# Kernel tuning notes

Measured on AMD Instinct MI355X. Metric: run time of the kernel, lower is better.

## Reference

```python
import jax, jax.numpy as jnp
import numpy as np

N_NODES = 50000
N_EDGES = 800000
F_IN = 11
HID = 128
HEADS = 4
N_ACT = 6
NEG_SLOPE = 0.2


def _gat_layer(x, W, a_src, a_dst, b, src, dst, heads, out_dim):
    # x: [N, Fin]; W: [Fin, heads*out]; a_src/a_dst: [heads, out]; b: [heads*out]
    N = x.shape[0]
    h = (x @ W).reshape(N, heads, out_dim)                     # [N,H,C]
    alpha_src = jnp.einsum('nhc,hc->nh', h, a_src)             # [N,H]
    alpha_dst = jnp.einsum('nhc,hc->nh', h, a_dst)             # [N,H]
    e = jax.nn.leaky_relu(alpha_src[src] + alpha_dst[dst], NEG_SLOPE)  # [E,H]
    # segment softmax over incoming edges of each dst node
    m = jax.ops.segment_max(e, dst, num_segments=N)            # [N,H]
    ex = jnp.exp(e - m[dst])
    s = jax.ops.segment_sum(ex, dst, num_segments=N)           # [N,H]
    alpha = ex / s[dst]                                        # [E,H]
    msg = h[src] * alpha[..., None]                            # [E,H,C]
    agg = jax.ops.segment_sum(msg, dst, num_segments=N)        # [N,H,C]
    return agg.reshape(N, heads * out_dim) + b


def setup_inputs() -> dict:
    key = jax.random.key(0)
    ks = jax.random.split(key, 24)
    f32 = jnp.float32
    p = {}
    p['x'] = jax.random.normal(ks[0], (N_NODES, F_IN), dtype=f32)
    p['edge_index'] = jax.random.randint(ks[1], (2, N_EDGES), 0, N_NODES, dtype=jnp.int64)
    p['current_node_idx'] = 0
    def w(k, shape):
        return (jax.random.normal(k, shape, dtype=f32) * 0.1)
    p['W1'] = w(ks[2], (F_IN, HEADS * HID)); p['as1'] = w(ks[3], (HEADS, HID))
    p['ad1'] = w(ks[4], (HEADS, HID)); p['b1'] = jnp.zeros((HEADS * HID,), f32)
    p['W2'] = w(ks[5], (HEADS * HID, HEADS * HID)); p['as2'] = w(ks[6], (HEADS, HID))
    p['ad2'] = w(ks[7], (HEADS, HID)); p['b2'] = jnp.zeros((HEADS * HID,), f32)
    # layer 3: 512 -> 128, 1 head
    p['W3'] = w(ks[8], (HEADS * HID, HID)); p['as3'] = w(ks[9], (1, HID))
    p['ad3'] = w(ks[10], (1, HID)); p['b3'] = jnp.zeros((HID,), f32)
    # policy head
    p['pw1'] = w(ks[11], (HID, HID)); p['pb1'] = jnp.zeros((HID,), f32)
    p['pw2'] = w(ks[12], (HID, N_ACT)); p['pb2'] = jnp.zeros((N_ACT,), f32)
    # value head
    p['vw1'] = w(ks[13], (HID, HID)); p['vb1'] = jnp.zeros((HID,), f32)
    p['vw2'] = w(ks[14], (HID, 1)); p['vb2'] = jnp.zeros((1,), f32)
    return p


def reference(x, edge_index, current_node_idx,
              W1, as1, ad1, b1, W2, as2, ad2, b2, W3, as3, ad3, b3,
              pw1, pb1, pw2, pb2, vw1, vb1, vw2, vb2):
    src, dst = edge_index[0], edge_index[1]
    h = _gat_layer(x, W1, as1, ad1, b1, src, dst, HEADS, HID)
    h = jax.nn.elu(h)
    h = _gat_layer(h, W2, as2, ad2, b2, src, dst, HEADS, HID)
    h = jax.nn.elu(h)
    h = _gat_layer(h, W3, as3, ad3, b3, src, dst, 1, HID)      # [N, HID]
    graph_emb = h.mean(axis=0, keepdims=True)                  # [1, HID]
    combined = graph_emb + h[current_node_idx]                 # [1, HID]
    p = jax.nn.relu(combined @ pw1 + pb1) @ pw2 + pb2          # [1, N_ACT]
    v = jax.nn.relu(combined @ vw1 + vb1) @ vw2 + vb2          # [1, 1]
    return p, v
```

## Files before the change

kernel.cpp:

```cpp
#include <hip/hip_runtime.h>
#include <math.h>

#define NN 50000
#define NE 800000
#define F_IN 11
#define HID 128
#define NEG_SLOPE 0.2f

typedef __attribute__((ext_vector_type(8))) short short8;
typedef __attribute__((ext_vector_type(4))) float f32x4;

__device__ __forceinline__ float bf2f(ushort u) {
  return __uint_as_float(((unsigned)u) << 16);
}
__device__ __forceinline__ ushort f2bf(float f) {
  unsigned u = __float_as_uint(f);
  return (ushort)((u + 0x7fff + ((u >> 16) & 1)) >> 16);
}
__device__ __forceinline__ float lrelu(float x) { return x > 0.f ? x : NEG_SLOPE * x; }
__device__ __forceinline__ float elu1(float x) { return x > 0.f ? x : expm1f(x); }

#define MNEG (-1e30f)

__device__ __forceinline__ void wave_fence() {
  asm volatile("s_waitcnt lgkmcnt(0)" ::: "memory");
}

#define AS1 __attribute__((address_space(1)))
#define AS3 __attribute__((address_space(3)))

__global__ void k_deg(const int* __restrict__ ei, int* __restrict__ deg) {
  int e = blockIdx.x * blockDim.x + threadIdx.x;
  if (e < NE) atomicAdd(&deg[ei[NE + e]], 1);
}

__global__ void k_scan(const int* __restrict__ deg, int* __restrict__ row_ptr,
                       int* __restrict__ cursor) {
  const int T = 1024;
  const int CH = (NN + T - 1) / T;
  __shared__ int ssum[T];
  int t = threadIdx.x;
  int base = t * CH;
  int s = 0;
  for (int i = 0; i < CH; i++) {
    int idx = base + i;
    if (idx < NN) s += deg[idx];
  }
  ssum[t] = s;
  __syncthreads();
  for (int off = 1; off < T; off <<= 1) {
    int v = (t >= off) ? ssum[t - off] : 0;
    __syncthreads();
    ssum[t] += v;
    __syncthreads();
  }
  int run = ssum[t] - s;
  for (int i = 0; i < CH; i++) {
    int idx = base + i;
    if (idx < NN) {
      row_ptr[idx] = run;
      cursor[idx] = run;
      run += deg[idx];
    }
  }
  if (t == 0) row_ptr[NN] = ssum[T - 1];
}

__global__ void k_scatter(const int* __restrict__ ei, int* __restrict__ cursor,
                          int* __restrict__ csr_src) {
  int e = blockIdx.x * blockDim.x + threadIdx.x;
  if (e < NE) {
    int d = ei[NE + e];
    int pos = atomicAdd(&cursor[d], 1);
    csr_src[pos] = ei[e];
  }
}

__global__ void k_wt(const float* __restrict__ W, ushort* __restrict__ Wt, int K, int N) {
  __shared__ float tl[32][33];
  int bn = blockIdx.x * 32, bk = blockIdx.y * 32;
  int tx = threadIdx.x & 31, ty = threadIdx.x >> 5;
  for (int i = ty; i < 32; i += 8) tl[i][tx] = W[(size_t)(bk + i) * N + bn + tx];
  __syncthreads();
  for (int i = ty; i < 32; i += 8)
    Wt[(size_t)(bn + i) * K + bk + tx] = f2bf(tl[tx][i]);
}

__global__ void k_vsd(const float* __restrict__ W1, const float* __restrict__ as1,
                      const float* __restrict__ ad1, float* __restrict__ vs,
                      float* __restrict__ vd) {
  int t = threadIdx.x;
  if (t >= 88) return;
  int side = t & 1, kh = t >> 1;
  int k = kh >> 2, h = kh & 3;
  const float* av = side ? ad1 : as1;
  float s = 0.f;
  for (int c = 0; c < HID; c++) s += W1[k * 512 + h * HID + c] * av[h * HID + c];
  (side ? vd : vs)[kh] = s;
}

__global__ void k_ax(const float* __restrict__ x, const float* __restrict__ vs,
                     const float* __restrict__ vd, float* __restrict__ asrc,
                     float* __restrict__ adst) {
  int n = blockIdx.x * blockDim.x + threadIdx.x;
  if (n >= NN) return;
  float xr[F_IN];
#pragma unroll
  for (int k = 0; k < F_IN; k++) xr[k] = x[n * F_IN + k];
  float s[4] = {}, dd[4] = {};
#pragma unroll
  for (int k = 0; k < F_IN; k++)
#pragma unroll
    for (int h = 0; h < 4; h++) {
      s[h] += xr[k] * vs[k * 4 + h];
      dd[h] += xr[k] * vd[k * 4 + h];
    }
  *(f32x4*)(asrc + n * 4) = f32x4{s[0], s[1], s[2], s[3]};
  *(f32x4*)(adst + n * 4) = f32x4{dd[0], dd[1], dd[2], dd[3]};
}

__global__ __launch_bounds__(256) void k_aggpre(
    const float* __restrict__ x, const float* __restrict__ asrc,
    const float* __restrict__ adst, const int* __restrict__ row_ptr,
    const int* __restrict__ csr_src, float* __restrict__ P) {
  const int CAP = 64;
  __shared__ int src_c[4][CAP];
  __shared__ float ea[4][CAP * 4];
  int t = threadIdx.x, lane = t & 63, wv = t >> 6;
  int d = blockIdx.x * 4 + wv;
  int start = row_ptr[d], deg = row_ptr[d + 1] - start;
  int dcap = min(deg, CAP);
  for (int i = lane; i < dcap; i += 64) src_c[wv][i] = csr_src[start + i];
  wave_fence();
  int hh = lane & 3;
  float adh = adst[d * 4 + hh];
  float m = MNEG, s = 0.f;
  int deg4 = deg * 4;
  for (int i = lane; i < deg4; i += 64) {
    int k = i >> 2;
    int sn = (k < CAP) ? src_c[wv][k] : csr_src[start + k];
    float v = lrelu(asrc[sn * 4 + hh] + adh);
    if (k < CAP) ea[wv][i] = v;
    float nm = fmaxf(m, v);
    s = s * __expf(m - nm) + __expf(v - nm);
    m = nm;
  }
#pragma unroll
  for (int off = 4; off < 64; off <<= 1) {
    float m2 = __shfl_xor(m, off);
    float s2 = __shfl_xor(s, off);
    float nm = fmaxf(m, m2);
    s = s * __expf(m - nm) + s2 * __expf(m2 - nm);
    m = nm;
  }
  float sinv = (s > 0.f) ? 1.f / s : 0.f;
  int dc4 = dcap * 4;
  for (int i = lane; i < dc4; i += 64) ea[wv][i] = __expf(ea[wv][i] - m) * sinv;
  wave_fence();
  int hq = lane / F_IN;
  int k = lane - hq * F_IN;
  int h = hq & 3;
  float mh = __shfl(m, h), sih = __shfl(sinv, h);
  float adh2 = adst[d * 4 + h];
  float acc = 0.f;
#define GETP(i, SN, A)                                                \
  do {                                                                \
    int kk_ = e + (i);                                                \
    if (kk_ < CAP) {                                                  \
      SN = src_c[wv][kk_];                                            \
      A = ea[wv][kk_ * 4 + h];                                        \
    } else {                                                          \
      SN = csr_src[start + kk_];                                      \
      A = __expf(lrelu(asrc[SN * 4 + h] + adh2) - mh) * sih;          \
    }                                                                 \
  } while (0)
  int e = 0;
  for (; e + 4 <= deg; e += 4) {
    int sn0, sn1, sn2, sn3;
    float a0, a1, a2, a3;
    GETP(0, sn0, a0);
    GETP(1, sn1, a1);
    GETP(2, sn2, a2);
    GETP(3, sn3, a3);
    float x0 = x[sn0 * F_IN + k];
    float x1 = x[sn1 * F_IN + k];
    float x2 = x[sn2 * F_IN + k];
    float x3 = x[sn3 * F_IN + k];
    acc += a0 * x0 + a1 * x1 + a2 * x2 + a3 * x3;
  }
  for (; e < deg; e++) {
    int sn;
    float a;
    GETP(0, sn, a);
    acc += a * x[sn * F_IN + k];
  }
#undef GETP
  if (lane < 44) P[(size_t)d * 44 + lane] = acc;
}

__global__ __launch_bounds__(256) void k_gemm_l1(
    const float* __restrict__ P, const float* __restrict__ W1,
    const float* __restrict__ b1, ushort* __restrict__ out) {
  __shared__ float sW[F_IN * 512];
  __shared__ float sP[64][44];
  int t = threadIdx.x;
  for (int i = t; i < F_IN * 512; i += 256) sW[i] = W1[i];
  int n0 = blockIdx.x * 64;
  for (int i = t; i < 64 * 44; i += 256) {
    int nn = i / 44, kk = i % 44;
    sP[nn][kk] = (n0 + nn < NN) ? P[(size_t)(n0 + nn) * 44 + kk] : 0.f;
  }
  __syncthreads();
  int j0 = 2 * t;
  int h = j0 >> 7;
  float b0 = b1[j0], bb = b1[j0 + 1];
  float w0[F_IN], w1v[F_IN];
#pragma unroll
  for (int k = 0; k < F_IN; k++) {
    w0[k] = sW[k * 512 + j0];
    w1v[k] = sW[k * 512 + j0 + 1];
  }
  for (int nn = 0; nn < 64; nn++) {
    if (n0 + nn >= NN) break;
    float a0 = b0, a1 = bb;
#pragma unroll
    for (int k = 0; k < F_IN; k++) {
      float pv = sP[nn][h * F_IN + k];
      a0 += pv * w0[k];
      a1 += pv * w1v[k];
    }
    a0 = elu1(a0);
    a1 = elu1(a1);
    unsigned pk = (unsigned)f2bf(a0) | ((unsigned)f2bf(a1) << 16);
    *(unsigned*)(out + (size_t)(n0 + nn) * 512 + j0) = pk;
  }
}

#define TM 128
#define TN 128
#define TK 64
__global__ __launch_bounds__(256) void k_mfma(const ushort* __restrict__ A,
                                              const ushort* __restrict__ Bt,
                                              ushort* __restrict__ C,
                                              int M, int N, int K, int H) {
  __shared__ ushort lds[TM * TK + TN * TK];
  ushort* As = lds;
  ushort* Bs = lds + TM * TK;
  int tid = threadIdx.x;
  int lane = tid & 63, wv = tid >> 6;
  int wr = wv >> 1, wc = wv & 1;
  int nwg = gridDim.x;
  int q = nwg >> 3, rr = nwg & 7;
  int xcd = blockIdx.x & 7, off8 = blockIdx.x >> 3;
  int lid = (xcd < rr ? xcd * (q + 1) : rr * (q + 1) + (xcd - rr) * q) + off8;
  int bm = lid / H, hy = lid - bm * H;
  int bm0 = bm * TM, bn0 = hy * TN;
  int l15 = lane & 15, l4 = lane >> 4;
  f32x4 acc[4][4] = {};
  for (int k0 = 0; k0 < K; k0 += TK) {
#pragma unroll
    for (int it = 0; it < 4; ++it) {
      int chunk = it * 4 + wv;
      int pbase = chunk * 1024;
      int p = pbase + lane * 16;
      int prow = p >> 7;
      int lblk = ((p >> 4) & 7) ^ (prow & 7);
      int gr = bm0 + prow;
      gr = gr < M ? gr : M - 1;
      __builtin_amdgcn_global_load_lds(
          (const AS1 void*)(A + (size_t)gr * K + (k0 + lblk * 8)),
          (AS3 void*)((char*)As + pbase), 16, 0, 0);
      int gb = bn0 + prow;
      __builtin_amdgcn_global_load_lds(
          (const AS1 void*)(Bt + (size_t)gb * K + (k0 + lblk * 8)),
          (AS3 void*)((char*)Bs + pbase), 16, 0, 0);
    }
    __syncthreads();
#pragma unroll
    for (int kk = 0; kk < 2; ++kk) {
      int cb = kk * 4 + l4;
      short8 af[4], bfr[4];
#pragma unroll
      for (int m = 0; m < 4; ++m) {
        int row = wr * 64 + m * 16 + l15;
        af[m] = *(const short8*)((const char*)As + row * 128 + ((cb ^ (row & 7)) << 4));
      }
#pragma unroll
      for (int n = 0; n < 4; ++n) {
        int row = wc * 64 + n * 16 + l15;
        bfr[n] = *(const short8*)((const char*)Bs + row * 128 + ((cb ^ (row & 7)) << 4));
      }
#pragma unroll
      for (int m = 0; m < 4; ++m)
#pragma unroll
        for (int n = 0; n < 4; ++n)
          acc[m][n] = __builtin_amdgcn_mfma_f32_16x16x32_bf16(af[m], bfr[n], acc[m][n], 0, 0, 0);
    }
    __syncthreads();
  }
#pragma unroll
  for (int m = 0; m < 4; ++m) {
#pragma unroll
    for (int r = 0; r < 4; ++r) {
      int row = bm0 + wr * 64 + m * 16 + l4 * 4 + r;
      if (row < M) {
#pragma unroll
        for (int n = 0; n < 4; ++n) {
          int col = bn0 + wc * 64 + n * 16 + l15;
          C[(size_t)row * N + col] = f2bf(acc[m][n][r]);
        }
      }
    }
  }
}

template <int H>
__global__ void k_alpha(const ushort* __restrict__ h, const float* __restrict__ a_src,
                        const float* __restrict__ a_dst, float* __restrict__ asrc,
                        float* __restrict__ adst) {
  int t = threadIdx.x;
  int lane = t & 63;
  int n_g, h_g;
  if (H == 4) {
    n_g = blockIdx.x * 4 + (t >> 6);
    h_g = lane >> 4;
  } else {
    n_g = blockIdx.x * 16 + (t >> 4);
    h_g = 0;
  }
  if (n_g >= NN) return;
  int cl = lane & 15;
  short8 hv = *(const short8*)(h + (size_t)n_g * (H * 128) + h_g * 128 + cl * 8);
  const float* as = a_src + h_g * 128 + cl * 8;
  const float* ad = a_dst + h_g * 128 + cl * 8;
  float s1 = 0.f, s2 = 0.f;
#pragma unroll
  for (int j = 0; j < 8; j++) {
    float v = bf2f((ushort)hv[j]);
    s1 += v * as[j];
    s2 += v * ad[j];
  }
#pragma unroll
  for (int off = 1; off < 16; off <<= 1) {
    s1 += __shfl_xor(s1, off);
    s2 += __shfl_xor(s2, off);
  }
  if (cl == 0) {
    asrc[n_g * H + h_g] = s1;
    adst[n_g * H + h_g] = s2;
  }
}

__global__ __launch_bounds__(256) void k_agg4w(
    const ushort* __restrict__ h, const float* __restrict__ asrc,
    const float* __restrict__ adst, const int* __restrict__ row_ptr,
    const int* __restrict__ csr_src, const float* __restrict__ bias,
    ushort* __restrict__ out) {
  const int CAP = 64;
  __shared__ int src_c[4][CAP];
  __shared__ float ea[4][CAP * 4];
  int t = threadIdx.x, lane = t & 63, wv = t >> 6;
  int d = blockIdx.x * 4 + wv;
  int start = row_ptr[d], deg = row_ptr[d + 1] - start;
  int dcap = min(deg, CAP);
  for (int i = lane; i < dcap; i += 64) src_c[wv][i] = csr_src[start + i];
  wave_fence();
  int hh = lane & 3;
  float adh = adst[d * 4 + hh];
  float m = MNEG, s = 0.f;
  int deg4 = deg * 4;
  for (int i = lane; i < deg4; i += 64) {
    int k = i >> 2;
    int sn = (k < CAP) ? src_c[wv][k] : csr_src[start + k];
    float v = lrelu(asrc[sn * 4 + hh] + adh);
    if (k < CAP) ea[wv][i] = v;
    float nm = fmaxf(m, v);
    s = s * __expf(m - nm) + __expf(v - nm);
    m = nm;
  }
#pragma unroll
  for (int off = 4; off < 64; off <<= 1) {
    float m2 = __shfl_xor(m, off);
    float s2 = __shfl_xor(s, off);
    float nm = fmaxf(m, m2);
    s = s * __expf(m - nm) + s2 * __expf(m2 - nm);
    m = nm;
  }
  float sinv = (s > 0.f) ? 1.f / s : 0.f;
  int dc4 = dcap * 4;
  for (int i = lane; i < dc4; i += 64) ea[wv][i] = __expf(ea[wv][i] - m) * sinv;
  wave_fence();
  int hl = lane >> 4;
  float mh = __shfl(m, hl), sih = __shfl(sinv, hl);
  float adh2 = adst[d * 4 + hl];
  float acc0[8] = {}, acc1[8] = {};
  int k = 0;
  for (; k + 2 <= deg; k += 2) {
    int sn0, sn1;
    float a0, a1;
    if (k < CAP) {
      sn0 = src_c[wv][k];
      a0 = ea[wv][k * 4 + hl];
    } else {
      sn0 = csr_src[start + k];
      a0 = __expf(lrelu(asrc[sn0 * 4 + hl] + adh2) - mh) * sih;
    }
    if (k + 1 < CAP) {
      sn1 = src_c[wv][k + 1];
      a1 = ea[wv][(k + 1) * 4 + hl];
    } else {
      sn1 = csr_src[start + k + 1];
      a1 = __expf(lrelu(asrc[sn1 * 4 + hl] + adh2) - mh) * sih;
    }
    short8 v0 = *(const short8*)(h + (size_t)sn0 * 512 + lane * 8);
    short8 v1 = *(const short8*)(h + (size_t)sn1 * 512 + lane * 8);
#pragma unroll
    for (int j = 0; j < 8; j++) acc0[j] += a0 * bf2f((ushort)v0[j]);
#pragma unroll
    for (int j = 0; j < 8; j++) acc1[j] += a1 * bf2f((ushort)v1[j]);
  }
  if (k < deg) {
    int sn;
    float a;
    if (k < CAP) {
      sn = src_c[wv][k];
      a = ea[wv][k * 4 + hl];
    } else {
      sn = csr_src[start + k];
      a = __expf(lrelu(asrc[sn * 4 + hl] + adh2) - mh) * sih;
    }
    short8 v0 = *(const short8*)(h + (size_t)sn * 512 + lane * 8);
#pragma unroll
    for (int j = 0; j < 8; j++) acc0[j] += a * bf2f((ushort)v0[j]);
  }
  const float* bp = bias + lane * 8;
  unsigned pk[4];
#pragma unroll
  for (int j = 0; j < 4; j++) {
    float o0 = elu1(acc0[2 * j] + acc1[2 * j] + bp[2 * j]);
    float o1 = elu1(acc0[2 * j + 1] + acc1[2 * j + 1] + bp[2 * j + 1]);
    pk[j] = (unsigned)f2bf(o0) | ((unsigned)f2bf(o1) << 16);
  }
  *(uint4*)(out + (size_t)d * 512 + lane * 8) = make_uint4(pk[0], pk[1], pk[2], pk[3]);
}

__global__ __launch_bounds__(256) void k_agg1w(
    const ushort* __restrict__ h, const float* __restrict__ asrc,
    const float* __restrict__ adst, const int* __restrict__ row_ptr,
    const int* __restrict__ csr_src, const float* __restrict__ bias,
    ushort* __restrict__ out) {
  const int CAP = 64;
  __shared__ int src_c[4][CAP];
  __shared__ float ea[4][CAP];
  int t = threadIdx.x, lane = t & 63, wv = t >> 6;
  int slot = lane >> 4, cl = lane & 15;
  int d = blockIdx.x * 4 + wv;
  int start = row_ptr[d], deg = row_ptr[d + 1] - start;
  int dcap = min(deg, CAP);
  for (int i = lane; i < dcap; i += 64) src_c[wv][i] = csr_src[start + i];
  wave_fence();
  float adh = adst[d];
  float m = MNEG, s = 0.f;
  for (int i = lane; i < deg; i += 64) {
    int sn = (i < CAP) ? src_c[wv][i] : csr_src[start + i];
    float v = lrelu(asrc[sn] + adh);
    if (i < CAP) ea[wv][i] = v;
    float nm = fmaxf(m, v);
    s = s * __expf(m - nm) + __expf(v - nm);
    m = nm;
  }
#pragma unroll
  for (int off = 1; off < 64; off <<= 1) {
    float m2 = __shfl_xor(m, off);
    float s2 = __shfl_xor(s, off);
    float nm = fmaxf(m, m2);
    s = s * __expf(m - nm) + s2 * __expf(m2 - nm);
    m = nm;
  }
  float sinv = (s > 0.f) ? 1.f / s : 0.f;
  for (int i = lane; i < dcap; i += 64) ea[wv][i] = __expf(ea[wv][i] - m) * sinv;
  wave_fence();
#define GET1(KK, SN, A)                                               \
  do {                                                                \
    if ((KK) < CAP) {                                                 \
      SN = src_c[wv][KK];                                             \
      A = ea[wv][KK];                                                 \
    } else {                                                          \
      SN = csr_src[start + (KK)];                                     \
      A = __expf(lrelu(asrc[SN] + adh) - m) * sinv;                   \
    }                                                                 \
  } while (0)
  float acc0[8] = {}, acc1[8] = {};
  int k = slot;
  for (; k + 4 < deg; k += 8) {
    int sn0, sn1;
    float a0, a1;
    GET1(k, sn0, a0);
    GET1(k + 4, sn1, a1);
    short8 v0 = *(const short8*)(h + (size_t)sn0 * 128 + cl * 8);
    short8 v1 = *(const short8*)(h + (size_t)sn1 * 128 + cl * 8);
#pragma unroll
    for (int j = 0; j < 8; j++) acc0[j] += a0 * bf2f((ushort)v0[j]);
#pragma unroll
    for (int j = 0; j < 8; j++) acc1[j] += a1 * bf2f((ushort)v1[j]);
  }
  for (; k < deg; k += 4) {
    int sn;
    float a;
    GET1(k, sn, a);
    short8 v0 = *(const short8*)(h + (size_t)sn * 128 + cl * 8);
#pragma unroll
    for (int j = 0; j < 8; j++) acc0[j] += a * bf2f((ushort)v0[j]);
  }
#undef GET1
#pragma unroll
  for (int j = 0; j < 8; j++) {
    float v = acc0[j] + acc1[j];
    v += __shfl_xor(v, 16);
    v += __shfl_xor(v, 32);
    acc0[j] = v;
  }
  if (slot == 0) {
    const float* bp = bias + cl * 8;
    unsigned pk[4];
#pragma unroll
    for (int j = 0; j < 4; j++) {
      float o0 = acc0[2 * j] + bp[2 * j];
      float o1 = acc0[2 * j + 1] + bp[2 * j + 1];
      pk[j] = (unsigned)f2bf(o0) | ((unsigned)f2bf(o1) << 16);
    }
    *(uint4*)(out + (size_t)d * 128 + cl * 8) = make_uint4(pk[0], pk[1], pk[2], pk[3]);
  }
}

__global__ __launch_bounds__(256) void k_colsum(const ushort* __restrict__ h3,
                                                float* __restrict__ gsum) {
  __shared__ float partial[16 * 128];
  int t = threadIdx.x;
  int rg = t >> 4, cl = t & 15;
  int nb = gridDim.x;
  int per = (NN + nb - 1) / nb;
  int r0 = blockIdx.x * per, r1 = min(NN, r0 + per);
  float acc[8] = {};
  for (int r = r0 + rg; r < r1; r += 16) {
    short8 hv = *(const short8*)(h3 + (size_t)r * 128 + cl * 8);
#pragma unroll
    for (int j = 0; j < 8; j++) acc[j] += bf2f((ushort)hv[j]);
  }
#pragma unroll
  for (int j = 0; j < 8; j++) partial[rg * 128 + cl * 8 + j] = acc[j];
  __syncthreads();
  if (t < 128) {
    float s = 0.f;
    for (int q = 0; q < 16; q++) s += partial[q * 128 + t];
    atomicAdd(&gsum[t], s);
  }
}

__global__ void k_head(const float* __restrict__ gsum, const ushort* __restrict__ h3,
                       const int* __restrict__ curp, const float* __restrict__ pw1,
                       const float* __restrict__ pb1, const float* __restrict__ pw2,
                       const float* __restrict__ pb2, const float* __restrict__ vw1,
                       const float* __restrict__ vb1, const float* __restrict__ vw2,
                       const float* __restrict__ vb2, float* __restrict__ outp) {
  __shared__ float comb[HID], ph[HID], vh[HID];
  int t = threadIdx.x;
  int cur = curp[0];
  comb[t] = gsum[t] * (1.f / NN) + bf2f(h3[(size_t)cur * HID + t]);
  __syncthreads();
  float accp = pb1[t], accv = vb1[t];
  for (int k = 0; k < HID; k++) {
    float cv = comb[k];
    accp += cv * pw1[k * HID + t];
    accv += cv * vw1[k * HID + t];
  }
  ph[t] = fmaxf(accp, 0.f);
  vh[t] = fmaxf(accv, 0.f);
  __syncthreads();
  if (t < 6) {
    float a = pb2[t];
    for (int k = 0; k < HID; k++) a += ph[k] * pw2[k * 6 + t];
    outp[t] = a;
  }
  if (t == 6) {
    float a = vb2[0];
    for (int k = 0; k < HID; k++) a += vh[k] * vw2[k];
    outp[6] = a;
  }
}

extern "C" void kernel_launch(void* const* d_in, const int* in_sizes, int n_in,
                              void* d_out, int out_size, void* d_ws, size_t ws_size,
                              hipStream_t stream) {
  const float* x = (const float*)d_in[0];
  const int* ei = (const int*)d_in[1];
  const int* cur = (const int*)d_in[2];
  const float* W1 = (const float*)d_in[3];
  const float* as1 = (const float*)d_in[4];
  const float* ad1 = (const float*)d_in[5];
  const float* b1 = (const float*)d_in[6];
  const float* W2 = (const float*)d_in[7];
  const float* as2 = (const float*)d_in[8];
  const float* ad2 = (const float*)d_in[9];
  const float* b2 = (const float*)d_in[10];
  const float* W3 = (const float*)d_in[11];
  const float* as3 = (const float*)d_in[12];
  const float* ad3 = (const float*)d_in[13];
  const float* b3 = (const float*)d_in[14];
  const float* pw1 = (const float*)d_in[15];
  const float* pb1 = (const float*)d_in[16];
  const float* pw2 = (const float*)d_in[17];
  const float* pb2 = (const float*)d_in[18];
  const float* vw1 = (const float*)d_in[19];
  const float* vb1 = (const float*)d_in[20];
  const float* vw2 = (const float*)d_in[21];
  const float* vb2 = (const float*)d_in[22];
  float* out = (float*)d_out;

  char* w = (char*)d_ws;
  ushort* G = (ushort*)w;    w += (size_t)NN * 512 * 2;
  ushort* Abuf = (ushort*)w; w += (size_t)NN * 512 * 2;
  ushort* Wt2 = (ushort*)w;  w += (size_t)512 * 512 * 2;
  ushort* Wt3 = (ushort*)w;  w += (size_t)128 * 512 * 2;
  float* P = (float*)w;      w += (size_t)NN * 44 * 4;
  float* asrc = (float*)w;   w += (size_t)NN * 4 * 4;
  float* adst = (float*)w;   w += (size_t)NN * 4 * 4;
  int* deg = (int*)w;        w += (size_t)NN * 4;
  int* cursor = (int*)w;     w += (size_t)NN * 4;
  int* row_ptr = (int*)w;    w += (size_t)(NN + 1) * 4;
  int* csr_src = (int*)w;    w += (size_t)NE * 4;
  float* gsum = (float*)w;   w += (size_t)HID * 4;
  float* vs = (float*)w;     w += 44 * 4;
  float* vd = (float*)w;     w += 44 * 4;

  hipMemsetAsync(deg, 0, NN * 4, stream);
  hipMemsetAsync(gsum, 0, HID * 4, stream);

  k_deg<<<(NE + 255) / 256, 256, 0, stream>>>(ei, deg);
  k_scan<<<1, 1024, 0, stream>>>(deg, row_ptr, cursor);
  k_scatter<<<(NE + 255) / 256, 256, 0, stream>>>(ei, cursor, csr_src);

  k_wt<<<dim3(512 / 32, 512 / 32), 256, 0, stream>>>(W2, Wt2, 512, 512);
  k_wt<<<dim3(128 / 32, 512 / 32), 256, 0, stream>>>(W3, Wt3, 512, 128);

  const int GB = (NN + TM - 1) / TM;

  k_vsd<<<1, 128, 0, stream>>>(W1, as1, ad1, vs, vd);
  k_ax<<<(NN + 255) / 256, 256, 0, stream>>>(x, vs, vd, asrc, adst);
  k_aggpre<<<NN / 4, 256, 0, stream>>>(x, asrc, adst, row_ptr, csr_src, P);
  k_gemm_l1<<<(NN + 63) / 64, 256, 0, stream>>>(P, W1, b1, Abuf);

  k_mfma<<<GB * 4, 256, 0, stream>>>(Abuf, Wt2, G, NN, 512, 512, 4);
  k_alpha<4><<<(NN + 3) / 4, 256, 0, stream>>>(G, as2, ad2, asrc, adst);
  k_agg4w<<<NN / 4, 256, 0, stream>>>(G, asrc, adst, row_ptr, csr_src, b2, Abuf);

  k_mfma<<<GB, 256, 0, stream>>>(Abuf, Wt3, G, NN, 128, 512, 1);
  k_alpha<1><<<(NN + 15) / 16, 256, 0, stream>>>(G, as3, ad3, asrc, adst);
  k_agg1w<<<NN / 4, 256, 0, stream>>>(G, asrc, adst, row_ptr, csr_src, b3, Abuf);

  k_colsum<<<256, 256, 0, stream>>>(Abuf, gsum);
  k_head<<<1, 128, 0, stream>>>(gsum, Abuf, cur, pw1, pb1, pw2, pb2, vw1, vb1, vw2, vb2, out);
}
```

Measured before the change: 668.0 us.

## Fuse prep, layer-1 projection and column-sum into neighbouring kernels to cut launches

Merges the weight transposes and the buffer zeroing into one prep kernel that replaces two memsets. Folds the small attention-vector computation into the per-node alpha kernel, and the layer-1 dense projection plus ELU into the aggregation kernel, so the P intermediate buffer is no longer written and read back. Also replaces the separate column-sum kernel with atomic accumulation into 64 partial rows inside the last aggregation, which the head kernel then reduces. The aim is fewer launches and less memory traffic. The cost is that every aggregation block now reloads the 22 KB W1 tile into LDS, and the last layer issues many atomics.

Result: slower. 949.3 us (+42.1%).

```diff
diff --git a/kernel.cpp b/kernel.cpp
--- a/kernel.cpp
+++ b/kernel.cpp
@@ -28,6 +28,36 @@
 
 #define AS1 __attribute__((address_space(1)))
 #define AS3 __attribute__((address_space(3)))
+
+__global__ __launch_bounds__(256) void k_prep(const float* __restrict__ W2,
+                                              const float* __restrict__ W3,
+                                              ushort* __restrict__ Wt2,
+                                              ushort* __restrict__ Wt3,
+                                              int* __restrict__ deg,
+                                              float* __restrict__ gpart) {
+  __shared__ float tl[32][33];
+  int b = blockIdx.x, t = threadIdx.x;
+  int tx = t & 31, ty = t >> 5;
+  if (b < 256) {
+    int bn = (b & 15) * 32, bk = (b >> 4) * 32;
+    for (int i = ty; i < 32; i += 8) tl[i][tx] = W2[(size_t)(bk + i) * 512 + bn + tx];
+    __syncthreads();
+    for (int i = ty; i < 32; i += 8)
+      Wt2[(size_t)(bn + i) * 512 + bk + tx] = f2bf(tl[tx][i]);
+  } else if (b < 320) {
+    int bb = b - 256;
+    int bn = (bb & 3) * 32, bk = (bb >> 2) * 32;
+    for (int i = ty; i < 32; i += 8) tl[i][tx] = W3[(size_t)(bk + i) * 128 + bn + tx];
+    __syncthreads();
+    for (int i = ty; i < 32; i += 8)
+      Wt3[(size_t)(bn + i) * 512 + bk + tx] = f2bf(tl[tx][i]);
+  } else {
+    int b2 = b - 320;
+    int idx = b2 * 256 + t;
+    if (idx < NN) deg[idx] = 0;
+    if (b2 < 32) gpart[b2 * 256 + t] = 0.f;
+  }
+}
 
 __global__ void k_deg(const int* __restrict__ ei, int* __restrict__ deg) {
   int e = blockIdx.x * blockDim.x + threadIdx.x;
@@ -76,33 +106,27 @@
   }
 }
 
-__global__ void k_wt(const float* __restrict__ W, ushort* __restrict__ Wt, int K, int N) {
-  __shared__ float tl[32][33];
-  int bn = blockIdx.x * 32, bk = blockIdx.y * 32;
-  int tx = threadIdx.x & 31, ty = threadIdx.x >> 5;
-  for (int i = ty; i < 32; i += 8) tl[i][tx] = W[(size_t)(bk + i) * N + bn + tx];
+__global__ __launch_bounds__(256) void k_axv(const float* __restrict__ x,
+                                             const float* __restrict__ W1,
+                                             const float* __restrict__ as1,
+                                             const float* __restrict__ ad1,
+                                             float* __restrict__ asrc,
+                                             float* __restrict__ adst) {
+  __shared__ float svs[44], svd[44];
+  int t = threadIdx.x;
+  if (t < 88) {
+    int side = t & 1, kh = t >> 1;
+    int k = kh >> 2, h = kh & 3;
+    const float* av = side ? ad1 : as1;
+    float s = 0.f;
+    for (int c = 0; c < HID; c++) s += W1[k * 512 + h * HID + c] * av[h * HID + c];
+    if (side)
+      svd[kh] = s;
+    else
+      svs[kh] = s;
+  }
   __syncthreads();
-  for (int i = ty; i < 32; i += 8)
-    Wt[(size_t)(bn + i) * K + bk + tx] = f2bf(tl[tx][i]);
-}
-
-__global__ void k_vsd(const float* __restrict__ W1, const float* __restrict__ as1,
-                      const float* __restrict__ ad1, float* __restrict__ vs,
-                      float* __restrict__ vd) {
-  int t = threadIdx.x;
-  if (t >= 88) return;
-  int side = t & 1, kh = t >> 1;
-  int k = kh >> 2, h = kh & 3;
-  const float* av = side ? ad1 : as1;
-  float s = 0.f;
-  for (int c = 0; c < HID; c++) s += W1[k * 512 + h * HID + c] * av[h * HID + c];
-  (side ? vd : vs)[kh] = s;
-}
-
-__global__ void k_ax(const float* __restrict__ x, const float* __restrict__ vs,
-                     const float* __restrict__ vd, float* __restrict__ asrc,
-                     float* __restrict__ adst) {
-  int n = blockIdx.x * blockDim.x + threadIdx.x;
+  int n = blockIdx.x * 256 + t;
   if (n >= NN) return;
   float xr[F_IN];
 #pragma unroll
@@ -112,8 +136,8 @@
   for (int k = 0; k < F_IN; k++)
 #pragma unroll
     for (int h = 0; h < 4; h++) {
-      s[h] += xr[k] * vs[k * 4 + h];
-      dd[h] += xr[k] * vd[k * 4 + h];
+      s[h] += xr[k] * svs[k * 4 + h];
+      dd[h] += xr[k] * svd[k * 4 + h];
     }
   *(f32x4*)(asrc + n * 4) = f32x4{s[0], s[1], s[2], s[3]};
   *(f32x4*)(adst + n * 4) = f32x4{dd[0], dd[1], dd[2], dd[3]};
@@ -122,11 +146,15 @@
 __global__ __launch_bounds__(256) void k_aggpre(
     const float* __restrict__ x, const float* __restrict__ asrc,
     const float* __restrict__ adst, const int* __restrict__ row_ptr,
-    const int* __restrict__ csr_src, float* __restrict__ P) {
+    const int* __restrict__ csr_src, const float* __restrict__ W1,
+    const float* __restrict__ b1, ushort* __restrict__ out) {
   const int CAP = 64;
+  __shared__ float sW[F_IN * 512];
   __shared__ int src_c[4][CAP];
   __shared__ float ea[4][CAP * 4];
+  __shared__ float sP[4][44];
   int t = threadIdx.x, lane = t & 63, wv = t >> 6;
+  for (int i = t; i < F_IN * 512; i += 256) sW[i] = W1[i];
   int d = blockIdx.x * 4 + wv;
   int start = row_ptr[d], deg = row_ptr[d + 1] - start;
   int dcap = min(deg, CAP);
@@ -195,45 +223,38 @@
     acc += a * x[sn * F_IN + k];
   }
 #undef GETP
-  if (lane < 44) P[(size_t)d * 44 + lane] = acc;
-}
-
-__global__ __launch_bounds__(256) void k_gemm_l1(
-    const float* __restrict__ P, const float* __restrict__ W1,
-    const float* __restrict__ b1, ushort* __restrict__ out) {
-  __shared__ float sW[F_IN * 512];
-  __shared__ float sP[64][44];
-  int t = threadIdx.x;
-  for (int i = t; i < F_IN * 512; i += 256) sW[i] = W1[i];
-  int n0 = blockIdx.x * 64;
-  for (int i = t; i < 64 * 44; i += 256) {
-    int nn = i / 44, kk = i % 44;
-    sP[nn][kk] = (n0 + nn < NN) ? P[(size_t)(n0 + nn) * 44 + kk] : 0.f;
-  }
+  if (lane < 44) sP[wv][lane] = acc;
   __syncthreads();
-  int j0 = 2 * t;
-  int h = j0 >> 7;
-  float b0 = b1[j0], bb = b1[j0 + 1];
-  float w0[F_IN], w1v[F_IN];
-#pragma unroll
-  for (int k = 0; k < F_IN; k++) {
-    w0[k] = sW[k * 512 + j0];
-    w1v[k] = sW[k * 512 + j0 + 1];
-  }
-  for (int nn = 0; nn < 64; nn++) {
-    if (n0 + nn >= NN) break;
-    float a0 = b0, a1 = bb;
-#pragma unroll
-    for (int k = 0; k < F_IN; k++) {
-      float pv = sP[nn][h * F_IN + k];
-      a0 += pv * w0[k];
-      a1 += pv * w1v[k];
-    }
-    a0 = elu1(a0);
-    a1 = elu1(a1);
-    unsigned pk = (unsigned)f2bf(a0) | ((unsigned)f2bf(a1) << 16);
-    *(unsigned*)(out + (size_t)(n0 + nn) * 512 + j0) = pk;
-  }
+  int j0 = lane * 8;
+  int hj = j0 >> 7;
+  float pv[F_IN];
+#pragma unroll
+  for (int kk = 0; kk < F_IN; kk++) pv[kk] = sP[wv][hj * F_IN + kk];
+  float o[8];
+#pragma unroll
+  for (int jj = 0; jj < 8; jj++) o[jj] = b1[j0 + jj];
+#pragma unroll
+  for (int kk = 0; kk < F_IN; kk++) {
+    float4 wa = *(const float4*)&sW[kk * 512 + j0];
+    float4 wb = *(const float4*)&sW[kk * 512 + j0 + 4];
+    float p = pv[kk];
+    o[0] += p * wa.x;
+    o[1] += p * wa.y;
+    o[2] += p * wa.z;
+    o[3] += p * wa.w;
+    o[4] += p * wb.x;
+    o[5] += p * wb.y;
+    o[6] += p * wb.z;
+    o[7] += p * wb.w;
+  }
+  unsigned pk[4];
+#pragma unroll
+  for (int j = 0; j < 4; j++) {
+    float e0 = elu1(o[2 * j]);
+    float e1 = elu1(o[2 * j + 1]);
+    pk[j] = (unsigned)f2bf(e0) | ((unsigned)f2bf(e1) << 16);
+  }
+  *(uint4*)(out + (size_t)d * 512 + j0) = make_uint4(pk[0], pk[1], pk[2], pk[3]);
 }
 
 #define TM 128
@@ -448,7 +469,7 @@
     const ushort* __restrict__ h, const float* __restrict__ asrc,
     const float* __restrict__ adst, const int* __restrict__ row_ptr,
     const int* __restrict__ csr_src, const float* __restrict__ bias,
-    ushort* __restrict__ out) {
+    ushort* __restrict__ out, float* __restrict__ gpart) {
   const int CAP = 64;
   __shared__ int src_c[4][CAP];
   __shared__ float ea[4][CAP];
@@ -522,42 +543,21 @@
   }
   if (slot == 0) {
     const float* bp = bias + cl * 8;
+    float ov[8];
+#pragma unroll
+    for (int j = 0; j < 8; j++) ov[j] = acc0[j] + bp[j];
     unsigned pk[4];
 #pragma unroll
-    for (int j = 0; j < 4; j++) {
-      float o0 = acc0[2 * j] + bp[2 * j];
-      float o1 = acc0[2 * j + 1] + bp[2 * j + 1];
-      pk[j] = (unsigned)f2bf(o0) | ((unsigned)f2bf(o1) << 16);
-    }
+    for (int j = 0; j < 4; j++)
+      pk[j] = (unsigned)f2bf(ov[2 * j]) | ((unsigned)f2bf(ov[2 * j + 1]) << 16);
     *(uint4*)(out + (size_t)d * 128 + cl * 8) = make_uint4(pk[0], pk[1], pk[2], pk[3]);
-  }
-}
-
-__global__ __launch_bounds__(256) void k_colsum(const ushort* __restrict__ h3,
-                                                float* __restrict__ gsum) {
-  __shared__ float partial[16 * 128];
-  int t = threadIdx.x;
-  int rg = t >> 4, cl = t & 15;
-  int nb = gridDim.x;
-  int per = (NN + nb - 1) / nb;
-  int r0 = blockIdx.x * per, r1 = min(NN, r0 + per);
-  float acc[8] = {};
-  for (int r = r0 + rg; r < r1; r += 16) {
-    short8 hv = *(const short8*)(h3 + (size_t)r * 128 + cl * 8);
-#pragma unroll
-    for (int j = 0; j < 8; j++) acc[j] += bf2f((ushort)hv[j]);
-  }
-#pragma unroll
-  for (int j = 0; j < 8; j++) partial[rg * 128 + cl * 8 + j] = acc[j];
-  __syncthreads();
-  if (t < 128) {
-    float s = 0.f;
-    for (int q = 0; q < 16; q++) s += partial[q * 128 + t];
-    atomicAdd(&gsum[t], s);
-  }
-}
-
-__global__ void k_head(const float* __restrict__ gsum, const ushort* __restrict__ h3,
+    float* gp = gpart + (blockIdx.x & 63) * 128 + cl * 8;
+#pragma unroll
+    for (int j = 0; j < 8; j++) atomicAdd(&gp[j], ov[j]);
+  }
+}
+
+__global__ void k_head(const float* __restrict__ gpart, const ushort* __restrict__ h3,
                        const int* __restrict__ curp, const float* __restrict__ pw1,
                        const float* __restrict__ pb1, const float* __restrict__ pw2,
                        const float* __restrict__ pb2, const float* __restrict__ vw1,
@@ -566,7 +566,10 @@
   __shared__ float comb[HID], ph[HID], vh[HID];
   int t = threadIdx.x;
   int cur = curp[0];
-  comb[t] = gsum[t] * (1.f / NN) + bf2f(h3[(size_t)cur * HID + t]);
+  float gs = 0.f;
+#pragma unroll 8
+  for (int r = 0; r < 64; r++) gs += gpart[r * 128 + t];
+  comb[t] = gs * (1.f / NN) + bf2f(h3[(size_t)cur * HID + t]);
   __syncthreads();
   float accp = pb1[t], accv = vb1[t];
   for (int k = 0; k < HID; k++) {
@@ -622,33 +625,24 @@
   ushort* Abuf = (ushort*)w; w += (size_t)NN * 512 * 2;
   ushort* Wt2 = (ushort*)w;  w += (size_t)512 * 512 * 2;
   ushort* Wt3 = (ushort*)w;  w += (size_t)128 * 512 * 2;
-  float* P = (float*)w;      w += (size_t)NN * 44 * 4;
   float* asrc = (float*)w;   w += (size_t)NN * 4 * 4;
   float* adst = (float*)w;   w += (size_t)NN * 4 * 4;
   int* deg = (int*)w;        w += (size_t)NN * 4;
   int* cursor = (int*)w;     w += (size_t)NN * 4;
   int* row_ptr = (int*)w;    w += (size_t)(NN + 1) * 4;
   int* csr_src = (int*)w;    w += (size_t)NE * 4;
-  float* gsum = (float*)w;   w += (size_t)HID * 4;
-  float* vs = (float*)w;     w += 44 * 4;
-  float* vd = (float*)w;     w += 44 * 4;
-
-  hipMemsetAsync(deg, 0, NN * 4, stream);
-  hipMemsetAsync(gsum, 0, HID * 4, stream);
+  float* gpart = (float*)w;  w += (size_t)64 * 128 * 4;
+
+  k_prep<<<516, 256, 0, stream>>>(W2, W3, Wt2, Wt3, deg, gpart);
 
   k_deg<<<(NE + 255) / 256, 256, 0, stream>>>(ei, deg);
   k_scan<<<1, 1024, 0, stream>>>(deg, row_ptr, cursor);
   k_scatter<<<(NE + 255) / 256, 256, 0, stream>>>(ei, cursor, csr_src);
 
-  k_wt<<<dim3(512 / 32, 512 / 32), 256, 0, stream>>>(W2, Wt2, 512, 512);
-  k_wt<<<dim3(128 / 32, 512 / 32), 256, 0, stream>>>(W3, Wt3, 512, 128);
-
   const int GB = (NN + TM - 1) / TM;
 
-  k_vsd<<<1, 128, 0, stream>>>(W1, as1, ad1, vs, vd);
-  k_ax<<<(NN + 255) / 256, 256, 0, stream>>>(x, vs, vd, asrc, adst);
-  k_aggpre<<<NN / 4, 256, 0, stream>>>(x, asrc, adst, row_ptr, csr_src, P);
-  k_gemm_l1<<<(NN + 63) / 64, 256, 0, stream>>>(P, W1, b1, Abuf);
+  k_axv<<<(NN + 255) / 256, 256, 0, stream>>>(x, W1, as1, ad1, asrc, adst);
+  k_aggpre<<<NN / 4, 256, 0, stream>>>(x, asrc, adst, row_ptr, csr_src, W1, b1, Abuf);
 
   k_mfma<<<GB * 4, 256, 0, stream>>>(Abuf, Wt2, G, NN, 512, 512, 4);
   k_alpha<4><<<(NN + 3) / 4, 256, 0, stream>>>(G, as2, ad2, asrc, adst);
@@ -656,8 +650,7 @@
 
   k_mfma<<<GB, 256, 0, stream>>>(Abuf, Wt3, G, NN, 128, 512, 1);
   k_alpha<1><<<(NN + 15) / 16, 256, 0, stream>>>(G, as3, ad3, asrc, adst);
-  k_agg1w<<<NN / 4, 256, 0, stream>>>(G, asrc, adst, row_ptr, csr_src, b3, Abuf);
-
-  k_colsum<<<256, 256, 0, stream>>>(Abuf, gsum);
-  k_head<<<1, 128, 0, stream>>>(gsum, Abuf, cur, pw1, pb1, pw2, pb2, vw1, vb1, vw2, vb2, out);
-}
+  k_agg1w<<<NN / 4, 256, 0, stream>>>(G, asrc, adst, row_ptr, csr_src, b3, Abuf, gpart);
+
+  k_head<<<1, 128, 0, stream>>>(gpart, Abuf, cur, pw1, pb1, pw2, pb2, vw1, vb1, vw2, vb2, out);
+}
```
